# Optimization experiments

Hardware: AMD Instinct MI355X
Metric: run time of the kernel (lower is better)

Reference implementation:

```python
import jax, jax.numpy as jnp
import numpy as np

NUM_FEATURES = 602
NUM_CLASSES = 41
HIDDEN = 8
HEADS1 = 8
HEADS2 = 1
N_NODES = 100000
N_EDGES = 1600000
NEG_SLOPE = 0.2  # PyG GATConv default leaky_relu slope
EPS = 1e-16      # PyG softmax denominator epsilon


def gat_conv(x, edge_index, W, att_src, att_dst, bias, heads, out_ch, concat):
    """Faithful PyG GATConv forward (eval mode, dropout disabled).
    x: [N, F_in], edge_index: [2, E] with row0=src, row1=dst.
    W: [F_in, heads*out_ch], att_src/att_dst: [heads, out_ch], bias: [heads*out_ch] or [out_ch].
    """
    N = x.shape[0]
    h = (x @ W).reshape(N, heads, out_ch)              # [N, H, C]
    a_src = jnp.einsum('nhc,hc->nh', h, att_src)       # [N, H]
    a_dst = jnp.einsum('nhc,hc->nh', h, att_dst)       # [N, H]
    src, dst = edge_index[0], edge_index[1]
    e = jax.nn.leaky_relu(a_src[src] + a_dst[dst], NEG_SLOPE)  # [E, H]
    # segment softmax over incoming edges of each dst node
    m = jax.ops.segment_max(e, dst, num_segments=N)    # [N, H]
    e = jnp.exp(e - m[dst])
    denom = jax.ops.segment_sum(e, dst, num_segments=N)  # [N, H]
    alpha = e / (denom[dst] + EPS)                     # [E, H]
    msg = h[src] * alpha[:, :, None]                   # [E, H, C]
    out = jax.ops.segment_sum(msg, dst, num_segments=N)  # [N, H, C]
    if concat:
        out = out.reshape(N, heads * out_ch)
    else:
        out = out.mean(axis=1)
    return out + bias


def setup_inputs() -> dict:
    key = jax.random.key(0)
    ks = jax.random.split(key, 10)
    x = jax.random.normal(ks[0], (N_NODES, NUM_FEATURES), dtype=jnp.float32)
    edge_index = jax.random.randint(ks[1], (2, N_EDGES), 0, N_NODES, dtype=jnp.int64)
    s = 0.1
    W1 = jax.random.normal(ks[2], (NUM_FEATURES, HEADS1 * HIDDEN), dtype=jnp.float32) * s
    att_src1 = jax.random.normal(ks[3], (HEADS1, HIDDEN), dtype=jnp.float32) * s
    att_dst1 = jax.random.normal(ks[4], (HEADS1, HIDDEN), dtype=jnp.float32) * s
    b1 = jnp.zeros((HEADS1 * HIDDEN,), dtype=jnp.float32)
    W2 = jax.random.normal(ks[5], (HEADS1 * HIDDEN, HEADS2 * NUM_CLASSES), dtype=jnp.float32) * s
    att_src2 = jax.random.normal(ks[6], (HEADS2, NUM_CLASSES), dtype=jnp.float32) * s
    att_dst2 = jax.random.normal(ks[7], (HEADS2, NUM_CLASSES), dtype=jnp.float32) * s
    b2 = jnp.zeros((NUM_CLASSES,), dtype=jnp.float32)
    return {"x": x, "edge_index": edge_index, "W1": W1, "att_src1": att_src1,
            "att_dst1": att_dst1, "b1": b1, "W2": W2, "att_src2": att_src2,
            "att_dst2": att_dst2, "b2": b2}


def reference(x, edge_index, W1, att_src1, att_dst1, b1, W2, att_src2, att_dst2, b2):
    # eval mode: all F.dropout calls are identity
    h = gat_conv(x, edge_index, W1, att_src1, att_dst1, b1, HEADS1, HIDDEN, concat=True)
    h = jax.nn.elu(h)
    h = gat_conv(h, edge_index, W2, att_src2, att_dst2, b2, HEADS2, NUM_CLASSES, concat=False)
    return jax.nn.log_softmax(h, axis=1)
```

## Files before the change

kernel.cpp:

```cpp
#include <hip/hip_runtime.h>
#include <math.h>

#define NN 100000
#define NE 1600000
#define F_IN 602
#define H1 8
#define C1 8
#define F_MID 64
#define NC 41
#define NEG_SLOPE 0.2f
#define WT_LD 608

#define LRELU(x) fmaxf((x), NEG_SLOPE * (x))

typedef __attribute__((ext_vector_type(8))) short short8;
typedef __attribute__((ext_vector_type(4))) float f32x4;

__device__ inline unsigned short f2bf(float f) {
    unsigned u = __builtin_bit_cast(unsigned, f);
    unsigned r = (u + 0x7FFFu + ((u >> 16) & 1u)) >> 16;
    return (unsigned short)r;
}

__global__ void zero_kernel(int4* __restrict__ p, int n4)
{
    int i = blockIdx.x * blockDim.x + threadIdx.x;
    if (i < n4) p[i] = make_int4(0, 0, 0, 0);
}

__global__ void prep_wt_kernel(const float* __restrict__ W, unsigned short* __restrict__ Wt)
{
    int idx = blockIdx.x * blockDim.x + threadIdx.x;
    if (idx >= F_MID * WT_LD) return;
    int col = idx / WT_LD, k = idx % WT_LD;
    Wt[idx] = (k < F_IN) ? f2bf(W[k * F_MID + col]) : (unsigned short)0;
}

__global__ __launch_bounds__(256) void gemm1_mfma(
    const float* __restrict__ x, const unsigned short* __restrict__ Wt,
    float* __restrict__ h, int N)
{
    __shared__ unsigned short As[128][40];
    __shared__ unsigned short Bs[64][40];

    int t = threadIdx.x;
    int lane = t & 63;
    int w = t >> 6;
    int l16 = lane & 15, lg = lane >> 4;
    int n0 = blockIdx.x * 128;

    int arow = t >> 1;
    int acol16 = (t & 1) * 16;
    const float* xrow = x + (size_t)(n0 + arow) * F_IN;
    bool rowok = (n0 + arow) < N;

    int bcol = t >> 2;
    int bk8 = (t & 3) * 8;

    f32x4 acc[2][4] = {};

    for (int k0 = 0; k0 < F_IN; k0 += 32) {
        unsigned short abuf[16];
        if (rowok && (k0 + 32 <= F_IN)) {
            #pragma unroll
            for (int i = 0; i < 8; ++i) {
                float2 v = *(const float2*)(xrow + k0 + acol16 + i * 2);
                abuf[i * 2]     = f2bf(v.x);
                abuf[i * 2 + 1] = f2bf(v.y);
            }
        } else {
            #pragma unroll
            for (int i = 0; i < 16; ++i) {
                int k = k0 + acol16 + i;
                abuf[i] = (rowok && k < F_IN) ? f2bf(xrow[k]) : (unsigned short)0;
            }
        }
        uint4 bvec = *(const uint4*)(Wt + (size_t)bcol * WT_LD + k0 + bk8);

        __syncthreads();
        *(uint4*)(&As[arow][acol16])     = *(uint4*)(&abuf[0]);
        *(uint4*)(&As[arow][acol16 + 8]) = *(uint4*)(&abuf[8]);
        *(uint4*)(&Bs[bcol][bk8])        = bvec;
        __syncthreads();

        short8 afrag[2], bfrag[4];
        #pragma unroll
        for (int m = 0; m < 2; ++m)
            afrag[m] = *(const short8*)(&As[w * 32 + m * 16 + l16][lg * 8]);
        #pragma unroll
        for (int n = 0; n < 4; ++n)
            bfrag[n] = *(const short8*)(&Bs[n * 16 + l16][lg * 8]);
        #pragma unroll
        for (int m = 0; m < 2; ++m)
            #pragma unroll
            for (int n = 0; n < 4; ++n)
                acc[m][n] = __builtin_amdgcn_mfma_f32_16x16x32_bf16(
                    afrag[m], bfrag[n], acc[m][n], 0, 0, 0);
    }

    #pragma unroll
    for (int m = 0; m < 2; ++m) {
        #pragma unroll
        for (int r = 0; r < 4; ++r) {
            int row = n0 + w * 32 + m * 16 + lg * 4 + r;
            if (row < N) {
                #pragma unroll
                for (int n = 0; n < 4; ++n)
                    h[(size_t)row * F_MID + n * 16 + l16] = acc[m][n][r];
            }
        }
    }
}

__global__ void attn1_kernel(const float* __restrict__ h,
                             const float* __restrict__ attS,
                             const float* __restrict__ attD,
                             float* __restrict__ asrc, float* __restrict__ adst, int N)
{
    int idx = blockIdx.x * blockDim.x + threadIdx.x;
    if (idx >= N * H1) return;
    int n = idx >> 3, hh = idx & 7;
    float s = 0.f, d = 0.f;
    #pragma unroll
    for (int c = 0; c < C1; ++c) {
        float v = h[n * F_MID + hh * C1 + c];
        s += v * attS[hh * C1 + c];
        d += v * attD[hh * C1 + c];
    }
    asrc[idx] = s;
    adst[idx] = d;
}

__global__ void deg_kernel(const int* __restrict__ dst, int* __restrict__ deg, int E)
{
    int e = blockIdx.x * blockDim.x + threadIdx.x;
    if (e < E) atomicAdd(&deg[dst[e]], 1);
}

__global__ void scan1_kernel(const int* __restrict__ deg, int* __restrict__ bsum, int N)
{
    int b = blockIdx.x, t = threadIdx.x;
    int base = b * 1024 + t * 16;
    int s = 0;
    #pragma unroll
    for (int i = 0; i < 16; ++i) { int idx = base + i; if (idx < N) s += deg[idx]; }
    #pragma unroll
    for (int o = 32; o > 0; o >>= 1) s += __shfl_down(s, o);
    if (t == 0) bsum[b] = s;
}

__global__ void scan2_kernel(const int* __restrict__ bsum, int* __restrict__ boff,
                             int nb, int* __restrict__ offs, int N, int E)
{
    __shared__ int buf[128];
    int t = threadIdx.x;
    int v = (t < nb) ? bsum[t] : 0;
    buf[t] = v;
    __syncthreads();
    for (int o = 1; o < 128; o <<= 1) {
        int u = (t >= o) ? buf[t - o] : 0;
        __syncthreads();
        buf[t] += u;
        __syncthreads();
    }
    if (t < nb) boff[t] = buf[t] - v;
    if (t == 0) offs[N] = E;
}

__global__ void scan3_kernel(const int* __restrict__ deg, const int* __restrict__ boff,
                             int* __restrict__ offs, int N)
{
    int b = blockIdx.x, t = threadIdx.x;
    int base = b * 1024 + t * 16;
    int loc[16];
    int s = 0;
    #pragma unroll
    for (int i = 0; i < 16; ++i) {
        int idx = base + i;
        loc[i] = (idx < N) ? deg[idx] : 0;
        s += loc[i];
    }
    int inc = s;
    #pragma unroll
    for (int o = 1; o < 64; o <<= 1) {
        int u = __shfl_up(inc, o);
        if (t >= o) inc += u;
    }
    int run = inc - s + boff[b];
    #pragma unroll
    for (int i = 0; i < 16; ++i) {
        int idx = base + i;
        if (idx < N) offs[idx] = run;
        run += loc[i];
    }
}

__global__ void scatter_kernel(const int* __restrict__ src, const int* __restrict__ dst,
                               const int* __restrict__ offs, int* __restrict__ cursor,
                               int* __restrict__ srcs, int E)
{
    int e = blockIdx.x * blockDim.x + threadIdx.x;
    if (e < E) {
        int d = dst[e];
        int pos = offs[d] + atomicAdd(&cursor[d], 1);
        srcs[pos] = src[e];
    }
}

__global__ void agg1_kernel(const int* __restrict__ offs, const int* __restrict__ srcs,
                            const float* __restrict__ h1,
                            const float* __restrict__ asrc, const float* __restrict__ adst,
                            const float* __restrict__ b1,
                            float* __restrict__ out1, int N)
{
    int wave = (blockIdx.x * blockDim.x + threadIdx.x) >> 6;
    int lane = threadIdx.x & 63;
    if (wave >= N) return;
    int n = wave;
    int hh = lane >> 3;
    int beg = offs[n], end = offs[n + 1];
    float ad = adst[n * H1 + hh];

    float m = -INFINITY, den = 0.f, acc = 0.f;
    int i = beg;
    for (; i + 4 <= end; i += 4) {
        int s0 = srcs[i], s1 = srcs[i + 1], s2 = srcs[i + 2], s3 = srcs[i + 3];
        float a0 = asrc[s0 * H1 + hh], a1 = asrc[s1 * H1 + hh];
        float a2 = asrc[s2 * H1 + hh], a3 = asrc[s3 * H1 + hh];
        float v0 = h1[s0 * F_MID + lane], v1 = h1[s1 * F_MID + lane];
        float v2 = h1[s2 * F_MID + lane], v3 = h1[s3 * F_MID + lane];
        float e0 = LRELU(a0 + ad), e1 = LRELU(a1 + ad);
        float e2 = LRELU(a2 + ad), e3 = LRELU(a3 + ad);
        float m4 = fmaxf(fmaxf(e0, e1), fmaxf(e2, e3));
        float mn = fmaxf(m, m4);
        float sc = __expf(m - mn);
        float p0 = __expf(e0 - mn), p1 = __expf(e1 - mn);
        float p2 = __expf(e2 - mn), p3 = __expf(e3 - mn);
        den = den * sc + ((p0 + p1) + (p2 + p3));
        acc = acc * sc + ((p0 * v0 + p1 * v1) + (p2 * v2 + p3 * v3));
        m = mn;
    }
    for (; i < end; ++i) {
        int s = srcs[i];
        float e = LRELU(asrc[s * H1 + hh] + ad);
        float hv = h1[s * F_MID + lane];
        float mn = fmaxf(m, e);
        float sc = __expf(m - mn);
        float p  = __expf(e - mn);
        den = den * sc + p;
        acc = acc * sc + p * hv;
        m = mn;
    }
    float inv = 1.f / (den + 1e-16f);
    float v = acc * inv + b1[lane];
    out1[n * F_MID + lane] = v > 0.f ? v : expm1f(v);
}

__global__ __launch_bounds__(256) void gemm2_kernel(
    const float* __restrict__ out1, const float* __restrict__ W2,
    float* __restrict__ h2, int N)
{
    __shared__ float ws[F_MID * NC];
    for (int i = threadIdx.x; i < F_MID * NC; i += 256) ws[i] = W2[i];
    __syncthreads();
    int idx = blockIdx.x * blockDim.x + threadIdx.x;
    if (idx >= N * NC) return;
    int n = idx / NC, j = idx % NC;
    const float* row = out1 + n * F_MID;
    float acc = 0.f;
    #pragma unroll
    for (int k = 0; k < F_MID; ++k) acc += row[k] * ws[k * NC + j];
    h2[idx] = acc;
}

__global__ void attn2_kernel(const float* __restrict__ h2,
                             const float* __restrict__ attS,
                             const float* __restrict__ attD,
                             float* __restrict__ asrc, float* __restrict__ adst, int N)
{
    int n = blockIdx.x * blockDim.x + threadIdx.x;
    if (n >= N) return;
    float s = 0.f, d = 0.f;
    #pragma unroll
    for (int j = 0; j < NC; ++j) {
        float v = h2[n * NC + j];
        s += v * attS[j];
        d += v * attD[j];
    }
    asrc[n] = s;
    adst[n] = d;
}

__global__ void agg2_kernel(const int* __restrict__ offs, const int* __restrict__ srcs,
                            const float* __restrict__ h2,
                            const float* __restrict__ asrc, const float* __restrict__ adst,
                            const float* __restrict__ b2,
                            float* __restrict__ out, int N)
{
    int wave = (blockIdx.x * blockDim.x + threadIdx.x) >> 6;
    int lane = threadIdx.x & 63;
    if (wave >= N) return;
    int n = wave;
    int beg = offs[n], end = offs[n + 1];
    float ad = adst[n];
    bool act = lane < NC;

    float m = -INFINITY, den = 0.f, acc = 0.f;
    int i = beg;
    for (; i + 4 <= end; i += 4) {
        int s0 = srcs[i], s1 = srcs[i + 1], s2 = srcs[i + 2], s3 = srcs[i + 3];
        float a0 = asrc[s0], a1 = asrc[s1], a2 = asrc[s2], a3 = asrc[s3];
        float v0 = act ? h2[s0 * NC + lane] : 0.f;
        float v1 = act ? h2[s1 * NC + lane] : 0.f;
        float v2 = act ? h2[s2 * NC + lane] : 0.f;
        float v3 = act ? h2[s3 * NC + lane] : 0.f;
        float e0 = LRELU(a0 + ad), e1 = LRELU(a1 + ad);
        float e2 = LRELU(a2 + ad), e3 = LRELU(a3 + ad);
        float m4 = fmaxf(fmaxf(e0, e1), fmaxf(e2, e3));
        float mn = fmaxf(m, m4);
        float sc = __expf(m - mn);
        float p0 = __expf(e0 - mn), p1 = __expf(e1 - mn);
        float p2 = __expf(e2 - mn), p3 = __expf(e3 - mn);
        den = den * sc + ((p0 + p1) + (p2 + p3));
        acc = acc * sc + ((p0 * v0 + p1 * v1) + (p2 * v2 + p3 * v3));
        m = mn;
    }
    for (; i < end; ++i) {
        int s = srcs[i];
        float e = LRELU(asrc[s] + ad);
        float hv = act ? h2[s * NC + lane] : 0.f;
        float mn = fmaxf(m, e);
        float sc = __expf(m - mn);
        float p  = __expf(e - mn);
        den = den * sc + p;
        acc = acc * sc + p * hv;
        m = mn;
    }
    float inv = 1.f / (den + 1e-16f);
    float v = act ? acc * inv + b2[lane] : -INFINITY;
    float mm = v;
    #pragma unroll
    for (int o = 32; o > 0; o >>= 1) mm = fmaxf(mm, __shfl_xor(mm, o));
    float ex = act ? __expf(v - mm) : 0.f;
    float S = ex;
    #pragma unroll
    for (int o = 32; o > 0; o >>= 1) S += __shfl_xor(S, o);
    if (act) out[n * NC + lane] = v - mm - logf(S);
}

extern "C" void kernel_launch(void* const* d_in, const int* in_sizes, int n_in,
                              void* d_out, int out_size, void* d_ws, size_t ws_size,
                              hipStream_t stream)
{
    const float* x     = (const float*)d_in[0];
    const int*   ei    = (const int*)  d_in[1];
    const float* W1    = (const float*)d_in[2];
    const float* attS1 = (const float*)d_in[3];
    const float* attD1 = (const float*)d_in[4];
    const float* b1    = (const float*)d_in[5];
    const float* W2    = (const float*)d_in[6];
    const float* attS2 = (const float*)d_in[7];
    const float* attD2 = (const float*)d_in[8];
    const float* b2    = (const float*)d_in[9];
    float* out = (float*)d_out;

    const int N = NN, E = NE;
    const int* src = ei;
    const int* dst = ei + E;

    char* p = (char*)d_ws;
    auto alloc = [&](size_t bytes) { char* r = p; p += (bytes + 255) & ~255ull; return r; };
    float* h1    = (float*)alloc((size_t)N * F_MID * 4);
    float* asrc1 = (float*)alloc((size_t)N * H1 * 4);
    float* adst1 = (float*)alloc((size_t)N * H1 * 4);
    float* out1  = (float*)alloc((size_t)N * F_MID * 4);
    float* h2    = (float*)alloc((size_t)N * NC * 4);
    float* asrc2 = (float*)alloc((size_t)N * 4);
    float* adst2 = (float*)alloc((size_t)N * 4);
    int*   deg   = (int*)alloc((size_t)2 * N * 4);
    int*   cursor= deg + N;
    int*   offs  = (int*)alloc((size_t)(N + 1) * 4);
    int*   srcs  = (int*)alloc((size_t)E * 4);
    unsigned short* Wt = (unsigned short*)alloc((size_t)F_MID * WT_LD * 2);
    const int NB = (N + 1023) / 1024;
    int*   bsum  = (int*)alloc((size_t)NB * 4);
    int*   boff  = (int*)alloc((size_t)NB * 4);

    const int n4 = (2 * N) / 4;
    zero_kernel<<<(n4 + 255) / 256, 256, 0, stream>>>((int4*)deg, n4);

    prep_wt_kernel<<<(F_MID * WT_LD + 255) / 256, 256, 0, stream>>>(W1, Wt);
    gemm1_mfma<<<(N + 127) / 128, 256, 0, stream>>>(x, Wt, h1, N);
    attn1_kernel<<<(N * H1 + 255) / 256, 256, 0, stream>>>(h1, attS1, attD1, asrc1, adst1, N);
    deg_kernel<<<(E + 255) / 256, 256, 0, stream>>>(dst, deg, E);
    scan1_kernel<<<NB, 64, 0, stream>>>(deg, bsum, N);
    scan2_kernel<<<1, 128, 0, stream>>>(bsum, boff, NB, offs, N, E);
    scan3_kernel<<<NB, 64, 0, stream>>>(deg, boff, offs, N);
    scatter_kernel<<<(E + 255) / 256, 256, 0, stream>>>(src, dst, offs, cursor, srcs, E);
    agg1_kernel<<<(N * 64 + 255) / 256, 256, 0, stream>>>(offs, srcs, h1, asrc1, adst1, b1, out1, N);
    gemm2_kernel<<<(N * NC + 255) / 256, 256, 0, stream>>>(out1, W2, h2, N);
    attn2_kernel<<<(N + 255) / 256, 256, 0, stream>>>(h2, attS2, attD2, asrc2, adst2, N);
    agg2_kernel<<<(N * 64 + 255) / 256, 256, 0, stream>>>(offs, srcs, h2, asrc2, adst2, b2, out, N);
}
```

Before: 486.8 us.

## Double K-tile to 64 and prefetch next tile into registers in gemm1

The first-layer GEMM now uses 64-wide K tiles instead of 32, halving the number of synchronised iterations. It also issues the global loads for the next tile into registers before running the MFMAs on the current shared-memory tile, so memory latency overlaps with compute. This costs more registers and shared memory per block, which may lower occupancy, and the padded weight stride grows to 640.

```diff
diff --git a/kernel.cpp b/kernel.cpp
--- a/kernel.cpp
+++ b/kernel.cpp
@@ -9,7 +9,8 @@
 #define F_MID 64
 #define NC 41
 #define NEG_SLOPE 0.2f
-#define WT_LD 608
+#define WT_LD 640
+#define NKT 10
 
 #define LRELU(x) fmaxf((x), NEG_SLOPE * (x))
 
@@ -40,8 +41,8 @@
     const float* __restrict__ x, const unsigned short* __restrict__ Wt,
     float* __restrict__ h, int N)
 {
-    __shared__ unsigned short As[128][40];
-    __shared__ unsigned short Bs[64][40];
+    __shared__ unsigned short As[128][72];
+    __shared__ unsigned short Bs[64][72];
 
     int t = threadIdx.x;
     int lane = t & 63;
@@ -50,52 +51,80 @@
     int n0 = blockIdx.x * 128;
 
     int arow = t >> 1;
-    int acol16 = (t & 1) * 16;
+    int ak0 = (t & 1) * 32;
     const float* xrow = x + (size_t)(n0 + arow) * F_IN;
     bool rowok = (n0 + arow) < N;
 
     int bcol = t >> 2;
-    int bk8 = (t & 3) * 8;
+    int bk0 = (t & 3) * 16;
+    const unsigned short* wrow = Wt + (size_t)bcol * WT_LD;
 
     f32x4 acc[2][4] = {};
-
-    for (int k0 = 0; k0 < F_IN; k0 += 32) {
-        unsigned short abuf[16];
-        if (rowok && (k0 + 32 <= F_IN)) {
+    float2 abuf[16];
+    uint4  bbuf[2];
+
+    {
+        #pragma unroll
+        for (int i = 0; i < 16; ++i) abuf[i] = *(const float2*)(xrow + ak0 + i * 2);
+        bbuf[0] = *(const uint4*)(wrow + bk0);
+        bbuf[1] = *(const uint4*)(wrow + bk0 + 8);
+        if (!rowok) {
             #pragma unroll
-            for (int i = 0; i < 8; ++i) {
-                float2 v = *(const float2*)(xrow + k0 + acol16 + i * 2);
-                abuf[i * 2]     = f2bf(v.x);
-                abuf[i * 2 + 1] = f2bf(v.y);
+            for (int i = 0; i < 16; ++i) abuf[i] = make_float2(0.f, 0.f);
+        }
+    }
+
+    for (int kt = 0; kt < NKT; ++kt) {
+        __syncthreads();
+        #pragma unroll
+        for (int i = 0; i < 4; ++i) {
+            unsigned short tmp[8];
+            #pragma unroll
+            for (int j = 0; j < 4; ++j) {
+                tmp[j * 2]     = f2bf(abuf[i * 4 + j].x);
+                tmp[j * 2 + 1] = f2bf(abuf[i * 4 + j].y);
             }
-        } else {
+            *(uint4*)(&As[arow][ak0 + i * 8]) = *(uint4*)tmp;
+        }
+        *(uint4*)(&Bs[bcol][bk0])     = bbuf[0];
+        *(uint4*)(&Bs[bcol][bk0 + 8]) = bbuf[1];
+        __syncthreads();
+
+        if (kt + 1 < NKT) {
+            int k0 = (kt + 1) * 64;
+            if (rowok && k0 + 64 <= F_IN) {
+                #pragma unroll
+                for (int i = 0; i < 16; ++i)
+                    abuf[i] = *(const float2*)(xrow + k0 + ak0 + i * 2);
+            } else {
+                #pragma unroll
+                for (int i = 0; i < 16; ++i) {
+                    int k = k0 + ak0 + i * 2;
+                    float a = (rowok && k < F_IN)     ? xrow[k]     : 0.f;
+                    float b = (rowok && k + 1 < F_IN) ? xrow[k + 1] : 0.f;
+                    abuf[i] = make_float2(a, b);
+                }
+            }
+            bbuf[0] = *(const uint4*)(wrow + k0 + bk0);
+            bbuf[1] = *(const uint4*)(wrow + k0 + bk0 + 8);
+        }
+
+        #pragma unroll
+        for (int ks = 0; ks < 2; ++ks) {
+            short8 afrag[2], bfrag[4];
             #pragma unroll
-            for (int i = 0; i < 16; ++i) {
-                int k = k0 + acol16 + i;
-                abuf[i] = (rowok && k < F_IN) ? f2bf(xrow[k]) : (unsigned short)0;
-            }
-        }
-        uint4 bvec = *(const uint4*)(Wt + (size_t)bcol * WT_LD + k0 + bk8);
-
-        __syncthreads();
-        *(uint4*)(&As[arow][acol16])     = *(uint4*)(&abuf[0]);
-        *(uint4*)(&As[arow][acol16 + 8]) = *(uint4*)(&abuf[8]);
-        *(uint4*)(&Bs[bcol][bk8])        = bvec;
-        __syncthreads();
-
-        short8 afrag[2], bfrag[4];
-        #pragma unroll
-        for (int m = 0; m < 2; ++m)
-            afrag[m] = *(const short8*)(&As[w * 32 + m * 16 + l16][lg * 8]);
-        #pragma unroll
-        for (int n = 0; n < 4; ++n)
-            bfrag[n] = *(const short8*)(&Bs[n * 16 + l16][lg * 8]);
-        #pragma unroll
-        for (int m = 0; m < 2; ++m)
+            for (int m = 0; m < 2; ++m)
+                afrag[m] = *(const short8*)(&As[w * 32 + m * 16 + l16][ks * 32 + lg * 8]);
             #pragma unroll
             for (int n = 0; n < 4; ++n)
-                acc[m][n] = __builtin_amdgcn_mfma_f32_16x16x32_bf16(
-                    afrag[m], bfrag[n], acc[m][n], 0, 0, 0);
+                bfrag[n] = *(const short8*)(&Bs[n * 16 + l16][ks * 32 + lg * 8]);
+            #pragma unroll
+            for (int m = 0; m < 2; ++m)
+                #pragma unroll
+                for (int n = 0; n < 4; ++n)
+                    acc[m][n] = __builtin_amdgcn_mfma_f32_16x16x32_bf16(
+                        afrag[m], bfrag[n], acc[m][n], 0, 0, 0);
+        }
     }
 
     #pragma unroll
```

Result: slower. 500.6 us (+2.8%).

## Load GEMM1 MFMA fragments directly from global memory, dropping LDS staging

Applied to the files above, without the earlier changes.

The first-layer GEMM no longer stages x and W tiles through shared memory with two barriers per k-step. Each lane now loads its own A and B fragments straight from global memory, converts them to bf16, and the k-loop is fully unrolled with a separate masked tail step. The padded W leading dimension grows to 640 so that the tail B loads stay in bounds. The aim is to remove LDS traffic and synchronisation, at the cost of less coalesced, strided per-lane x loads and redundant W reads across waves.

```diff
diff --git a/kernel.cpp b/kernel.cpp
--- a/kernel.cpp
+++ b/kernel.cpp
@@ -9,7 +9,7 @@
 #define F_MID 64
 #define NC 41
 #define NEG_SLOPE 0.2f
-#define WT_LD 608
+#define WT_LD 640
 
 #define LRELU(x) fmaxf((x), NEG_SLOPE * (x))
 
@@ -22,6 +22,19 @@
     return (unsigned short)r;
 }
 
+__device__ inline short8 load_cvt8(const float* __restrict__ p) {
+    float2 v0 = *(const float2*)(p);
+    float2 v1 = *(const float2*)(p + 2);
+    float2 v2 = *(const float2*)(p + 4);
+    float2 v3 = *(const float2*)(p + 6);
+    short8 r;
+    r[0] = (short)f2bf(v0.x); r[1] = (short)f2bf(v0.y);
+    r[2] = (short)f2bf(v1.x); r[3] = (short)f2bf(v1.y);
+    r[4] = (short)f2bf(v2.x); r[5] = (short)f2bf(v2.y);
+    r[6] = (short)f2bf(v3.x); r[7] = (short)f2bf(v3.y);
+    return r;
+}
+
 __global__ void zero_kernel(int4* __restrict__ p, int n4)
 {
     int i = blockIdx.x * blockDim.x + threadIdx.x;
@@ -40,69 +53,68 @@
     const float* __restrict__ x, const unsigned short* __restrict__ Wt,
     float* __restrict__ h, int N)
 {
-    __shared__ unsigned short As[128][40];
-    __shared__ unsigned short Bs[64][40];
-
     int t = threadIdx.x;
     int lane = t & 63;
     int w = t >> 6;
     int l16 = lane & 15, lg = lane >> 4;
-    int n0 = blockIdx.x * 128;
-
-    int arow = t >> 1;
-    int acol16 = (t & 1) * 16;
-    const float* xrow = x + (size_t)(n0 + arow) * F_IN;
-    bool rowok = (n0 + arow) < N;
-
-    int bcol = t >> 2;
-    int bk8 = (t & 3) * 8;
+    int row0 = blockIdx.x * 128 + w * 32;
+
+    int r0 = row0 + l16;
+    int r1 = row0 + 16 + l16;
+    const float* a0 = x + (size_t)(r0 < N ? r0 : 0) * F_IN + lg * 8;
+    const float* a1 = x + (size_t)(r1 < N ? r1 : 0) * F_IN + lg * 8;
+    const unsigned short* bp = Wt + (size_t)l16 * WT_LD + lg * 8;
 
     f32x4 acc[2][4] = {};
 
-    for (int k0 = 0; k0 < F_IN; k0 += 32) {
-        unsigned short abuf[16];
-        if (rowok && (k0 + 32 <= F_IN)) {
+    #pragma unroll
+    for (int kt = 0; kt < 9; ++kt) {
+        int k0 = kt * 64;
+        #pragma unroll
+        for (int ks = 0; ks < 2; ++ks) {
+            int ko = k0 + ks * 32;
+            short8 af0 = load_cvt8(a0 + ko);
+            short8 af1 = load_cvt8(a1 + ko);
+            short8 bf[4];
             #pragma unroll
-            for (int i = 0; i < 8; ++i) {
-                float2 v = *(const float2*)(xrow + k0 + acol16 + i * 2);
-                abuf[i * 2]     = f2bf(v.x);
-                abuf[i * 2 + 1] = f2bf(v.y);
-            }
-        } else {
+            for (int n = 0; n < 4; ++n)
+                bf[n] = *(const short8*)(bp + (size_t)n * 16 * WT_LD + ko);
             #pragma unroll
-            for (int i = 0; i < 16; ++i) {
-                int k = k0 + acol16 + i;
-                abuf[i] = (rowok && k < F_IN) ? f2bf(xrow[k]) : (unsigned short)0;
+            for (int n = 0; n < 4; ++n) {
+                acc[0][n] = __builtin_amdgcn_mfma_f32_16x16x32_bf16(af0, bf[n], acc[0][n], 0, 0, 0);
+                acc[1][n] = __builtin_amdgcn_mfma_f32_16x16x32_bf16(af1, bf[n], acc[1][n], 0, 0, 0);
             }
         }
-        uint4 bvec = *(const uint4*)(Wt + (size_t)bcol * WT_LD + k0 + bk8);
-
-        __syncthreads();
-        *(uint4*)(&As[arow][acol16])     = *(uint4*)(&abuf[0]);
-        *(uint4*)(&As[arow][acol16 + 8]) = *(uint4*)(&abuf[8]);
-        *(uint4*)(&Bs[bcol][bk8])        = bvec;
-        __syncthreads();
-
-        short8 afrag[2], bfrag[4];
-        #pragma unroll
-        for (int m = 0; m < 2; ++m)
-            afrag[m] = *(const short8*)(&As[w * 32 + m * 16 + l16][lg * 8]);
+    }
+    {
+        const int k0 = 576;
+        float v0[8], v1[8];
+        #pragma unroll
+        for (int i = 0; i < 8; ++i) {
+            int k = k0 + lg * 8 + i;
+            bool ok = k < F_IN;
+            v0[i] = ok ? a0[k0 + i] : 0.f;
+            v1[i] = ok ? a1[k0 + i] : 0.f;
+        }
+        short8 af0, af1;
+        #pragma unroll
+        for (int i = 0; i < 8; ++i) { af0[i] = (short)f2bf(v0[i]); af1[i] = (short)f2bf(v1[i]); }
+        short8 bf[4];
         #pragma unroll
         for (int n = 0; n < 4; ++n)
-            bfrag[n] = *(const short8*)(&Bs[n * 16 + l16][lg * 8]);
-        #pragma unroll
-        for (int m = 0; m < 2; ++m)
-            #pragma unroll
-            for (int n = 0; n < 4; ++n)
-                acc[m][n] = __builtin_amdgcn_mfma_f32_16x16x32_bf16(
-                    afrag[m], bfrag[n], acc[m][n], 0, 0, 0);
+            bf[n] = *(const short8*)(bp + (size_t)n * 16 * WT_LD + k0);
+        #pragma unroll
+        for (int n = 0; n < 4; ++n) {
+            acc[0][n] = __builtin_amdgcn_mfma_f32_16x16x32_bf16(af0, bf[n], acc[0][n], 0, 0, 0);
+            acc[1][n] = __builtin_amdgcn_mfma_f32_16x16x32_bf16(af1, bf[n], acc[1][n], 0, 0, 0);
+        }
     }
 
     #pragma unroll
     for (int m = 0; m < 2; ++m) {
         #pragma unroll
         for (int r = 0; r < 4; ++r) {
-            int row = n0 + w * 32 + m * 16 + lg * 4 + r;
+            int row = row0 + m * 16 + lg * 4 + r;
             if (row < N) {
                 #pragma unroll
                 for (int n = 0; n < 4; ++n)
```

New measurement: 509.5 us. 1.05x slower.

## Halve GEMM1 row tile and prefetch next K-tile into registers

Applied to the files above, without the earlier changes.

The first-layer bf16 MFMA GEMM now uses 64-row tiles instead of 128, which doubles the grid to about 1563 blocks. Each block software-prefetches the next K-slice of x and W into registers while the current slice is computed from shared memory. The padded W leading dimension grows to 640 so the last tile can read W unguarded. The aim is more memory-level parallelism and overlap of the x global loads, which dominate this memory-bound GEMM. In exchange, each staged B tile is reused over fewer rows and register use per thread rises.

```diff
diff --git a/kernel.cpp b/kernel.cpp
--- a/kernel.cpp
+++ b/kernel.cpp
@@ -9,7 +9,7 @@
 #define F_MID 64
 #define NC 41
 #define NEG_SLOPE 0.2f
-#define WT_LD 608
+#define WT_LD 640
 
 #define LRELU(x) fmaxf((x), NEG_SLOPE * (x))
 
@@ -40,74 +40,77 @@
     const float* __restrict__ x, const unsigned short* __restrict__ Wt,
     float* __restrict__ h, int N)
 {
-    __shared__ unsigned short As[128][40];
+    __shared__ unsigned short As[64][40];
     __shared__ unsigned short Bs[64][40];
 
     int t = threadIdx.x;
     int lane = t & 63;
     int w = t >> 6;
     int l16 = lane & 15, lg = lane >> 4;
-    int n0 = blockIdx.x * 128;
-
-    int arow = t >> 1;
-    int acol16 = (t & 1) * 16;
-    const float* xrow = x + (size_t)(n0 + arow) * F_IN;
-    bool rowok = (n0 + arow) < N;
-
+    int n0 = blockIdx.x * 64;
+
+    int arow = t >> 2, aseg = t & 3;
+    int grow = n0 + arow;
+    const float* xrow = x + (size_t)(grow < N ? grow : 0) * F_IN + aseg * 8;
     int bcol = t >> 2;
-    int bk8 = (t & 3) * 8;
-
-    f32x4 acc[2][4] = {};
-
-    for (int k0 = 0; k0 < F_IN; k0 += 32) {
-        unsigned short abuf[16];
-        if (rowok && (k0 + 32 <= F_IN)) {
+    const unsigned short* wrow = Wt + (size_t)bcol * WT_LD + aseg * 8;
+
+    f32x4 acc[4] = {};
+    float2 av[4];
+    uint4  bv;
+
+    #pragma unroll
+    for (int i = 0; i < 4; ++i) av[i] = *(const float2*)(xrow + i * 2);
+    bv = *(const uint4*)(wrow);
+
+    for (int kt = 0; kt < 19; ++kt) {
+        __syncthreads();
+        {
+            unsigned short tmp[8];
             #pragma unroll
-            for (int i = 0; i < 8; ++i) {
-                float2 v = *(const float2*)(xrow + k0 + acol16 + i * 2);
-                abuf[i * 2]     = f2bf(v.x);
-                abuf[i * 2 + 1] = f2bf(v.y);
+            for (int i = 0; i < 4; ++i) {
+                tmp[i * 2]     = f2bf(av[i].x);
+                tmp[i * 2 + 1] = f2bf(av[i].y);
             }
-        } else {
-            #pragma unroll
-            for (int i = 0; i < 16; ++i) {
-                int k = k0 + acol16 + i;
-                abuf[i] = (rowok && k < F_IN) ? f2bf(xrow[k]) : (unsigned short)0;
+            *(uint4*)(&As[arow][aseg * 8]) = *(uint4*)tmp;
+            *(uint4*)(&Bs[bcol][aseg * 8]) = bv;
+        }
+        __syncthreads();
+
+        if (kt < 18) {
+            int k0 = (kt + 1) * 32;
+            if (kt + 1 < 18) {
+                #pragma unroll
+                for (int i = 0; i < 4; ++i) av[i] = *(const float2*)(xrow + k0 + i * 2);
+            } else {
+                #pragma unroll
+                for (int i = 0; i < 4; ++i) {
+                    int k = k0 + aseg * 8 + i * 2;
+                    float a = (k < F_IN)     ? xrow[k0 + i * 2]     : 0.f;
+                    float b = (k + 1 < F_IN) ? xrow[k0 + i * 2 + 1] : 0.f;
+                    av[i] = make_float2(a, b);
+                }
             }
+            bv = *(const uint4*)(wrow + k0);
         }
-        uint4 bvec = *(const uint4*)(Wt + (size_t)bcol * WT_LD + k0 + bk8);
-
-        __syncthreads();
-        *(uint4*)(&As[arow][acol16])     = *(uint4*)(&abuf[0]);
-        *(uint4*)(&As[arow][acol16 + 8]) = *(uint4*)(&abuf[8]);
-        *(uint4*)(&Bs[bcol][bk8])        = bvec;
-        __syncthreads();
-
-        short8 afrag[2], bfrag[4];
-        #pragma unroll
-        for (int m = 0; m < 2; ++m)
-            afrag[m] = *(const short8*)(&As[w * 32 + m * 16 + l16][lg * 8]);
+
+        short8 afrag = *(const short8*)(&As[w * 16 + l16][lg * 8]);
+        short8 bfrag[4];
         #pragma unroll
         for (int n = 0; n < 4; ++n)
             bfrag[n] = *(const short8*)(&Bs[n * 16 + l16][lg * 8]);
         #pragma unroll
-        for (int m = 0; m < 2; ++m)
+        for (int n = 0; n < 4; ++n)
+            acc[n] = __builtin_amdgcn_mfma_f32_16x16x32_bf16(afrag, bfrag[n], acc[n], 0, 0, 0);
+    }
+
+    #pragma unroll
+    for (int r = 0; r < 4; ++r) {
+        int row = n0 + w * 16 + lg * 4 + r;
+        if (row < N) {
             #pragma unroll
             for (int n = 0; n < 4; ++n)
-                acc[m][n] = __builtin_amdgcn_mfma_f32_16x16x32_bf16(
-                    afrag[m], bfrag[n], acc[m][n], 0, 0, 0);
-    }
-
-    #pragma unroll
-    for (int m = 0; m < 2; ++m) {
-        #pragma unroll
-        for (int r = 0; r < 4; ++r) {
-            int row = n0 + w * 32 + m * 16 + lg * 4 + r;
-            if (row < N) {
-                #pragma unroll
-                for (int n = 0; n < 4; ++n)
-                    h[(size_t)row * F_MID + n * 16 + l16] = acc[m][n][r];
-            }
+                h[(size_t)row * F_MID + n * 16 + l16] = acc[n][r];
         }
     }
 }
@@ -390,7 +393,7 @@
     zero_kernel<<<(n4 + 255) / 256, 256, 0, stream>>>((int4*)deg, n4);
 
     prep_wt_kernel<<<(F_MID * WT_LD + 255) / 256, 256, 0, stream>>>(W1, Wt);
-    gemm1_mfma<<<(N + 127) / 128, 256, 0, stream>>>(x, Wt, h1, N);
+    gemm1_mfma<<<(N + 63) / 64, 256, 0, stream>>>(x, Wt, h1, N);
     attn1_kernel<<<(N * H1 + 255) / 256, 256, 0, stream>>>(h1, attS1, attD1, asrc1, adst1, N);
     deg_kernel<<<(E + 255) / 256, 256, 0, stream>>>(dst, deg, E);
     scan1_kernel<<<NB, 64, 0, stream>>>(deg, bsum, N);
```

Result: faster. 470.3 us (-3.4%).
